# Optimization experiments

Hardware: AMD Instinct MI355X
Metric: run time of the kernel (lower is better)

Reference implementation:

```python
import jax, jax.numpy as jnp
import numpy as np

T = 200000  # stack depth
V = 130     # vocab_size == input_dim
H = 512     # hid_dim
L = 2       # n_layers


def setup_inputs() -> dict:
    key = jax.random.key(0)
    ks = jax.random.split(key, 24)
    s = 0.05
    inp = {
        "input": jax.random.normal(ks[0], (1, 1, V), jnp.float32),
        "prev_Val": jax.random.normal(ks[1], (T, V), jnp.float32),
        "prev_stg": jax.random.uniform(ks[2], (T,), jnp.float32),
        "prev_read": jax.random.normal(ks[3], (V,), jnp.float32),
        "prev_h": jax.random.normal(ks[4], (L, 1, H), jnp.float32) * 0.1,
        "prev_c": jax.random.normal(ks[5], (L, 1, H), jnp.float32) * 0.1,
        # LSTM layer 0 (pytorch layout: W_ih (4H, in), W_hh (4H, H), gates i,f,g,o)
        "W_ih0": jax.random.normal(ks[6], (4 * H, V), jnp.float32) * s,
        "W_hh0": jax.random.normal(ks[7], (4 * H, H), jnp.float32) * s,
        "b_ih0": jax.random.normal(ks[8], (4 * H,), jnp.float32) * s,
        "b_hh0": jax.random.normal(ks[9], (4 * H,), jnp.float32) * s,
        # LSTM layer 1
        "W_ih1": jax.random.normal(ks[10], (4 * H, H), jnp.float32) * s,
        "W_hh1": jax.random.normal(ks[11], (4 * H, H), jnp.float32) * s,
        "b_ih1": jax.random.normal(ks[12], (4 * H,), jnp.float32) * s,
        "b_hh1": jax.random.normal(ks[13], (4 * H,), jnp.float32) * s,
        # gate heads (original inits these to zeros; random here to exercise math)
        "Wd": jax.random.normal(ks[14], (H,), jnp.float32) * s,
        "Bd": jax.random.normal(ks[15], (), jnp.float32) * s,
        "Wu": jax.random.normal(ks[16], (H,), jnp.float32) * s,
        "Bu": jax.random.normal(ks[17], (), jnp.float32) * s,
        "Wv": jax.random.normal(ks[18], (H, V), jnp.float32) * s,
        "Bv": jax.random.normal(ks[19], (V,), jnp.float32) * s,
        "Wo": jax.random.normal(ks[20], (H, H), jnp.float32) * s,
        "Bo": jax.random.normal(ks[21], (H,), jnp.float32) * s,
    }
    return inp


def _lstm_cell(x, h, c, Wih, Whh, bih, bhh):
    # x: (1, in), h/c: (1, H)
    g = x @ Wih.T + h @ Whh.T + bih + bhh  # (1, 4H)
    i, f, gg, o = jnp.split(g, 4, axis=-1)
    c2 = jax.nn.sigmoid(f) * c + jax.nn.sigmoid(i) * jnp.tanh(gg)
    h2 = jax.nn.sigmoid(o) * jnp.tanh(c2)
    return h2, c2


def reference(input, prev_Val, prev_stg, prev_read, prev_h, prev_c,
              W_ih0, W_hh0, b_ih0, b_hh0, W_ih1, W_hh1, b_ih1, b_hh1,
              Wd, Bd, Wu, Bu, Wv, Bv, Wo, Bo):
    x = (input + prev_read)[0]  # (1, V), seq_len == 1, batch == 1
    h1, c1 = _lstm_cell(x, prev_h[0], prev_c[0], W_ih0, W_hh0, b_ih0, b_hh0)
    h2, c2 = _lstm_cell(h1, prev_h[1], prev_c[1], W_ih1, W_hh1, b_ih1, b_hh1)
    output = h2  # (1, H)

    dt = jax.nn.sigmoid(output @ Wd + Bd)[0]      # scalar push strength
    ut = jax.nn.sigmoid(output @ Wu + Bu)[0]      # scalar pop strength
    vt = jnp.tanh(output @ Wv + Bv)               # (1, V) pushed value
    ot = jnp.tanh(output @ Wo + Bo)               # (1, H) controller output

    Val = jnp.concatenate([prev_Val, vt], axis=0)  # (T+1, V)

    # pop pass (top -> bottom): stg[i] = max(0, prev_stg[i] - max(0, ut)); ut -= stg[i]
    def pop_step(u, s):
        sn = jnp.maximum(0.0, s - jnp.maximum(0.0, u))
        return u - sn, sn
    _, stg_popped = jax.lax.scan(pop_step, ut, prev_stg, reverse=True)
    stg = jnp.concatenate([stg_popped, dt[None]])  # (T+1,)

    # read pass (top -> bottom): coef = min(stg[i], max(0, read)); read -= stg[i]
    def read_step(r, s):
        coef = jnp.minimum(s, jnp.maximum(0.0, r))
        return r - s, coef
    _, coefs = jax.lax.scan(read_step, jnp.asarray(1.0, stg.dtype), stg, reverse=True)
    rt = coefs @ Val  # (V,)

    h_new = jnp.stack([h1, h2])  # (L, 1, H)
    c_new = jnp.stack([c1, c2])
    return ot, Val, stg, rt, h_new, c_new
```

## Files before the change

### kernel.cpp

```cpp
#include <hip/hip_runtime.h>

#define T_DEPTH 200000
#define V_DIM   130
#define H_DIM   512

#define OT_OFF   0
#define VAL_OFF  512
#define STG_OFF  26000642
#define RT_OFF   26200643
#define HN_OFF   26200773
#define CN_OFF   26201797

#define WS_DTUT  0
#define WS_H1    64
#define WS_C1    576
#define WS_H2    1088
#define WS_C2    1600

#define NV4 6500000
#define NS2 100000

static __device__ __forceinline__ float sigmoidf_(float x) {
  return 1.0f / (1.0f + expf(-x));
}

__global__ void k_bulk(const float4* __restrict__ val_in,
                       const float2* __restrict__ stg_in,
                       float* __restrict__ out) {
  const int NT = NV4 + NS2;
  float4* __restrict__ val_out = reinterpret_cast<float4*>(out + VAL_OFF);
  float2* __restrict__ stg_out = reinterpret_cast<float2*>(out + STG_OFF);
  int stride = gridDim.x * blockDim.x;
  for (int u = blockIdx.x * blockDim.x + threadIdx.x; u < NT; u += stride) {
    if (u < NV4) val_out[u] = val_in[u];
    else { int s = u - NV4; stg_out[s] = stg_in[s]; }
  }
}

static __device__ __forceinline__ void lstm_unit(
    const float* __restrict__ Wih, int in_dim,
    const float* __restrict__ x_a, const float* __restrict__ x_b,
    const float* __restrict__ Whh, const float* __restrict__ hprev,
    const float* __restrict__ bih, const float* __restrict__ bhh,
    const float* __restrict__ cprev, int j, int lane,
    float* __restrict__ h_ws, float* __restrict__ c_ws,
    float* __restrict__ h_out, float* __restrict__ c_out) {
  float pg[4];
#pragma unroll
  for (int q = 0; q < 4; ++q) {
    int row = q * H_DIM + j;
    const float* wr = Wih + row * in_dim;
    const float* wh = Whh + row * H_DIM;
    float acc = 0.f;
    if (x_b) {
      for (int c = lane; c < in_dim; c += 64) acc += wr[c] * (x_a[c] + x_b[c]);
    } else {
      for (int c = lane; c < in_dim; c += 64) acc += wr[c] * x_a[c];
    }
    for (int k = lane; k < H_DIM; k += 64) acc += wh[k] * hprev[k];
    for (int off = 32; off; off >>= 1) acc += __shfl_down(acc, off, 64);
    pg[q] = acc;
  }
  if (lane == 0) {
    float ig = sigmoidf_(pg[0] + bih[j] + bhh[j]);
    float fg = sigmoidf_(pg[1] + bih[H_DIM + j] + bhh[H_DIM + j]);
    float gg = tanhf(pg[2] + bih[2 * H_DIM + j] + bhh[2 * H_DIM + j]);
    float og = sigmoidf_(pg[3] + bih[3 * H_DIM + j] + bhh[3 * H_DIM + j]);
    float cn = fg * cprev[j] + ig * gg;
    float hn = og * tanhf(cn);
    h_ws[j] = hn; c_ws[j] = cn;
    h_out[j] = hn; c_out[j] = cn;
  }
}

__global__ void kL0(const float* __restrict__ Wih, const float* __restrict__ Whh,
                    const float* __restrict__ bih, const float* __restrict__ bhh,
                    const float* __restrict__ inp, const float* __restrict__ prd,
                    const float* __restrict__ hprev, const float* __restrict__ cprev,
                    float* __restrict__ ws, float* __restrict__ out) {
  int j = blockIdx.x * 4 + (threadIdx.x >> 6), lane = threadIdx.x & 63;
  lstm_unit(Wih, V_DIM, inp, prd, Whh, hprev, bih, bhh, cprev, j, lane,
            ws + WS_H1, ws + WS_C1, out + HN_OFF, out + CN_OFF);
}

__global__ void kL1(const float* __restrict__ Wih, const float* __restrict__ Whh,
                    const float* __restrict__ bih, const float* __restrict__ bhh,
                    const float* __restrict__ hprev, const float* __restrict__ cprev,
                    float* __restrict__ ws, float* __restrict__ out) {
  int j = blockIdx.x * 4 + (threadIdx.x >> 6), lane = threadIdx.x & 63;
  lstm_unit(Wih, H_DIM, ws + WS_H1, nullptr, Whh, hprev, bih, bhh, cprev, j, lane,
            ws + WS_H2, ws + WS_C2, out + HN_OFF + H_DIM, out + CN_OFF + H_DIM);
}

__global__ void kheads(const float* __restrict__ Wv, const float* __restrict__ Bv,
                       const float* __restrict__ Wo, const float* __restrict__ Bo,
                       const float* __restrict__ Wd, const float* __restrict__ Bd,
                       const float* __restrict__ Wu, const float* __restrict__ Bu,
                       float* __restrict__ ws, float* __restrict__ out) {
  int bid = blockIdx.x, tid = threadIdx.x;
  const float* h2 = ws + WS_H2;
  if (bid < 2) {
    int t = bid * 256 + tid;
    float a0 = 0.f, a1 = 0.f, a2 = 0.f, a3 = 0.f;
    for (int k = 0; k < H_DIM; k += 4) {
      a0 += h2[k]     * Wo[k * H_DIM + t];
      a1 += h2[k + 1] * Wo[(k + 1) * H_DIM + t];
      a2 += h2[k + 2] * Wo[(k + 2) * H_DIM + t];
      a3 += h2[k + 3] * Wo[(k + 3) * H_DIM + t];
    }
    out[OT_OFF + t] = tanhf(((a0 + a1) + (a2 + a3)) + Bo[t]);
  } else if (bid == 2) {
    if (tid < V_DIM) {
      float a0 = 0.f, a1 = 0.f, a2 = 0.f, a3 = 0.f;
      for (int k = 0; k < H_DIM; k += 4) {
        a0 += h2[k]     * Wv[k * V_DIM + tid];
        a1 += h2[k + 1] * Wv[(k + 1) * V_DIM + tid];
        a2 += h2[k + 2] * Wv[(k + 2) * V_DIM + tid];
        a3 += h2[k + 3] * Wv[(k + 3) * V_DIM + tid];
      }
      out[VAL_OFF + T_DEPTH * V_DIM + tid] = tanhf(((a0 + a1) + (a2 + a3)) + Bv[tid]);
    }
  } else {
    int wid = tid >> 6, lane = tid & 63;
    if (wid < 2) {
      const float* wv = (wid == 0) ? Wd : Wu;
      float acc = 0.f;
      for (int k = lane; k < H_DIM; k += 64) acc += h2[k] * wv[k];
      for (int off = 32; off; off >>= 1) acc += __shfl_down(acc, off, 64);
      if (lane == 0) {
        if (wid == 0) {
          float dt = sigmoidf_(acc + Bd[0]);
          ws[WS_DTUT + 0] = dt;
          out[STG_OFF + T_DEPTH] = dt;
        } else {
          ws[WS_DTUT + 1] = sigmoidf_(acc + Bu[0]);
        }
      }
    }
  }
}

__global__ void ktop(const float* __restrict__ prev_stg, const float* __restrict__ prev_val,
                     const float* __restrict__ ws, float* __restrict__ out) {
  int t = threadIdx.x;
  float dt = ws[WS_DTUT + 0];
  float u  = ws[WS_DTUT + 1];
  float r  = 1.0f;
  float acc = 0.f;
  {
    float coef = fminf(dt, fmaxf(0.f, r));
    if (t < V_DIM) acc += coef * out[VAL_OFF + T_DEPTH * V_DIM + t];
    r -= dt;
  }
  for (int i = T_DEPTH - 1; i >= 0; --i) {
    bool pop_active = (u > 0.f);
    if (!pop_active && r <= 0.f) break;
    float s  = prev_stg[i];
    float sn = fmaxf(0.f, s - fmaxf(0.f, u));
    u -= sn;
    if (pop_active && t == 0) out[STG_OFF + i] = sn;
    float coef = fminf(sn, fmaxf(0.f, r));
    r -= sn;
    if (coef > 0.f && t < V_DIM) acc += coef * prev_val[i * V_DIM + t];
  }
  if (t < V_DIM) out[RT_OFF + t] = acc;
}

extern "C" void kernel_launch(void* const* d_in, const int* in_sizes, int n_in,
                              void* d_out, int out_size, void* d_ws, size_t ws_size,
                              hipStream_t stream) {
  (void)in_sizes; (void)n_in; (void)out_size; (void)ws_size;
  const float* input     = (const float*)d_in[0];
  const float* prev_Val  = (const float*)d_in[1];
  const float* prev_stg  = (const float*)d_in[2];
  const float* prev_read = (const float*)d_in[3];
  const float* prev_h    = (const float*)d_in[4];
  const float* prev_c    = (const float*)d_in[5];
  const float* W_ih0 = (const float*)d_in[6];
  const float* W_hh0 = (const float*)d_in[7];
  const float* b_ih0 = (const float*)d_in[8];
  const float* b_hh0 = (const float*)d_in[9];
  const float* W_ih1 = (const float*)d_in[10];
  const float* W_hh1 = (const float*)d_in[11];
  const float* b_ih1 = (const float*)d_in[12];
  const float* b_hh1 = (const float*)d_in[13];
  const float* Wd = (const float*)d_in[14];
  const float* Bd = (const float*)d_in[15];
  const float* Wu = (const float*)d_in[16];
  const float* Bu = (const float*)d_in[17];
  const float* Wv = (const float*)d_in[18];
  const float* Bv = (const float*)d_in[19];
  const float* Wo = (const float*)d_in[20];
  const float* Bo = (const float*)d_in[21];

  float* out = (float*)d_out;
  float* ws  = (float*)d_ws;

  k_bulk<<<4096, 256, 0, stream>>>((const float4*)prev_Val, (const float2*)prev_stg, out);
  kL0<<<128, 256, 0, stream>>>(W_ih0, W_hh0, b_ih0, b_hh0, input, prev_read,
                               prev_h, prev_c, ws, out);
  kL1<<<128, 256, 0, stream>>>(W_ih1, W_hh1, b_ih1, b_hh1,
                               prev_h + H_DIM, prev_c + H_DIM, ws, out);
  kheads<<<4, 256, 0, stream>>>(Wv, Bv, Wo, Bo, Wd, Bd, Wu, Bu, ws, out);
  ktop<<<1, 192, 0, stream>>>(prev_stg, prev_Val, ws, out);
}
```

Before: 307.9 us.

## Fuse head and stack-scan kernels; unroll bulk copy with nontemporal stores

The bulk copy of the value stack now uses 1024 blocks, an 8-way unrolled loop and nontemporal stores, meant to raise memory-level parallelism and avoid polluting the cache. The separate heads and stack-scan kernels are merged into one tail kernel. Its last block computes dt and ut with shared-memory reductions, recomputes vt locally and then runs the pop/read scan, which removes one launch and a workspace round trip. The price is that one block redundantly recomputes the vt projection, adding serial latency before the scan starts.

After: 314.9 us. 2.3% more time.

```diff
diff --git a/kernel.cpp b/kernel.cpp
--- a/kernel.cpp
+++ b/kernel.cpp
@@ -11,7 +11,6 @@
 #define HN_OFF   26200773
 #define CN_OFF   26201797
 
-#define WS_DTUT  0
 #define WS_H1    64
 #define WS_C1    576
 #define WS_H2    1088
@@ -19,22 +18,46 @@
 
 #define NV4 6500000
 #define NS2 100000
+#define CB  1024
+
+typedef float f32x4 __attribute__((ext_vector_type(4)));
+typedef float f32x2 __attribute__((ext_vector_type(2)));
 
 static __device__ __forceinline__ float sigmoidf_(float x) {
   return 1.0f / (1.0f + expf(-x));
 }
 
-__global__ void k_bulk(const float4* __restrict__ val_in,
-                       const float2* __restrict__ stg_in,
-                       float* __restrict__ out) {
-  const int NT = NV4 + NS2;
-  float4* __restrict__ val_out = reinterpret_cast<float4*>(out + VAL_OFF);
-  float2* __restrict__ stg_out = reinterpret_cast<float2*>(out + STG_OFF);
-  int stride = gridDim.x * blockDim.x;
-  for (int u = blockIdx.x * blockDim.x + threadIdx.x; u < NT; u += stride) {
-    if (u < NV4) val_out[u] = val_in[u];
-    else { int s = u - NV4; stg_out[s] = stg_in[s]; }
-  }
+__global__ void k_bulk8(const f32x4* __restrict__ vin,
+                        const f32x2* __restrict__ sin2,
+                        float* __restrict__ out) {
+  f32x4* __restrict__ vout = reinterpret_cast<f32x4*>(out + VAL_OFF);
+  const int S = gridDim.x * blockDim.x;
+  const int w = blockIdx.x * blockDim.x + threadIdx.x;
+  int u = w;
+  for (; u + 7 * S < NV4; u += 8 * S) {
+    f32x4 a0 = vin[u];
+    f32x4 a1 = vin[u + S];
+    f32x4 a2 = vin[u + 2 * S];
+    f32x4 a3 = vin[u + 3 * S];
+    f32x4 a4 = vin[u + 4 * S];
+    f32x4 a5 = vin[u + 5 * S];
+    f32x4 a6 = vin[u + 6 * S];
+    f32x4 a7 = vin[u + 7 * S];
+    __builtin_nontemporal_store(a0, vout + u);
+    __builtin_nontemporal_store(a1, vout + u + S);
+    __builtin_nontemporal_store(a2, vout + u + 2 * S);
+    __builtin_nontemporal_store(a3, vout + u + 3 * S);
+    __builtin_nontemporal_store(a4, vout + u + 4 * S);
+    __builtin_nontemporal_store(a5, vout + u + 5 * S);
+    __builtin_nontemporal_store(a6, vout + u + 6 * S);
+    __builtin_nontemporal_store(a7, vout + u + 7 * S);
+  }
+  for (; u < NV4; u += S) {
+    f32x4 a = vin[u];
+    __builtin_nontemporal_store(a, vout + u);
+  }
+  f32x2* __restrict__ sout = reinterpret_cast<f32x2*>(out + STG_OFF);
+  for (int v = w; v < NS2; v += S) sout[v] = sin2[v];
 }
 
 static __device__ __forceinline__ void lstm_unit(
@@ -92,11 +115,12 @@
             ws + WS_H2, ws + WS_C2, out + HN_OFF + H_DIM, out + CN_OFF + H_DIM);
 }
 
-__global__ void kheads(const float* __restrict__ Wv, const float* __restrict__ Bv,
-                       const float* __restrict__ Wo, const float* __restrict__ Bo,
-                       const float* __restrict__ Wd, const float* __restrict__ Bd,
-                       const float* __restrict__ Wu, const float* __restrict__ Bu,
-                       float* __restrict__ ws, float* __restrict__ out) {
+__global__ void ktail(const float* __restrict__ Wv, const float* __restrict__ Bv,
+                      const float* __restrict__ Wo, const float* __restrict__ Bo,
+                      const float* __restrict__ Wd, const float* __restrict__ Bd,
+                      const float* __restrict__ Wu, const float* __restrict__ Bu,
+                      const float* __restrict__ prev_stg, const float* __restrict__ prev_val,
+                      const float* __restrict__ ws, float* __restrict__ out) {
   int bid = blockIdx.x, tid = threadIdx.x;
   const float* h2 = ws + WS_H2;
   if (bid < 2) {
@@ -121,49 +145,62 @@
       out[VAL_OFF + T_DEPTH * V_DIM + tid] = tanhf(((a0 + a1) + (a2 + a3)) + Bv[tid]);
     }
   } else {
-    int wid = tid >> 6, lane = tid & 63;
-    if (wid < 2) {
-      const float* wv = (wid == 0) ? Wd : Wu;
-      float acc = 0.f;
-      for (int k = lane; k < H_DIM; k += 64) acc += h2[k] * wv[k];
-      for (int off = 32; off; off >>= 1) acc += __shfl_down(acc, off, 64);
-      if (lane == 0) {
-        if (wid == 0) {
-          float dt = sigmoidf_(acc + Bd[0]);
-          ws[WS_DTUT + 0] = dt;
-          out[STG_OFF + T_DEPTH] = dt;
-        } else {
-          ws[WS_DTUT + 1] = sigmoidf_(acc + Bu[0]);
-        }
+    __shared__ float red[256];
+    __shared__ float s_dt, s_ut;
+    float pd = h2[tid] * Wd[tid] + h2[tid + 256] * Wd[tid + 256];
+    float pu = h2[tid] * Wu[tid] + h2[tid + 256] * Wu[tid + 256];
+    red[tid] = pd;
+    __syncthreads();
+    for (int s = 128; s; s >>= 1) {
+      if (tid < s) red[tid] += red[tid + s];
+      __syncthreads();
+    }
+    if (tid == 0) s_dt = sigmoidf_(red[0] + Bd[0]);
+    __syncthreads();
+    red[tid] = pu;
+    __syncthreads();
+    for (int s = 128; s; s >>= 1) {
+      if (tid < s) red[tid] += red[tid + s];
+      __syncthreads();
+    }
+    if (tid == 0) s_ut = sigmoidf_(red[0] + Bu[0]);
+    __syncthreads();
+    float dt = s_dt;
+    float u  = s_ut;
+
+    float vt_local = 0.f;
+    if (tid < V_DIM) {
+      float a0 = 0.f, a1 = 0.f, a2 = 0.f, a3 = 0.f;
+      for (int k = 0; k < H_DIM; k += 4) {
+        a0 += h2[k]     * Wv[k * V_DIM + tid];
+        a1 += h2[k + 1] * Wv[(k + 1) * V_DIM + tid];
+        a2 += h2[k + 2] * Wv[(k + 2) * V_DIM + tid];
+        a3 += h2[k + 3] * Wv[(k + 3) * V_DIM + tid];
       }
-    }
-  }
-}
-
-__global__ void ktop(const float* __restrict__ prev_stg, const float* __restrict__ prev_val,
-                     const float* __restrict__ ws, float* __restrict__ out) {
-  int t = threadIdx.x;
-  float dt = ws[WS_DTUT + 0];
-  float u  = ws[WS_DTUT + 1];
-  float r  = 1.0f;
-  float acc = 0.f;
-  {
-    float coef = fminf(dt, fmaxf(0.f, r));
-    if (t < V_DIM) acc += coef * out[VAL_OFF + T_DEPTH * V_DIM + t];
-    r -= dt;
-  }
-  for (int i = T_DEPTH - 1; i >= 0; --i) {
-    bool pop_active = (u > 0.f);
-    if (!pop_active && r <= 0.f) break;
-    float s  = prev_stg[i];
-    float sn = fmaxf(0.f, s - fmaxf(0.f, u));
-    u -= sn;
-    if (pop_active && t == 0) out[STG_OFF + i] = sn;
-    float coef = fminf(sn, fmaxf(0.f, r));
-    r -= sn;
-    if (coef > 0.f && t < V_DIM) acc += coef * prev_val[i * V_DIM + t];
-  }
-  if (t < V_DIM) out[RT_OFF + t] = acc;
+      vt_local = tanhf(((a0 + a1) + (a2 + a3)) + Bv[tid]);
+    }
+    if (tid == 0) out[STG_OFF + T_DEPTH] = dt;
+
+    float r = 1.0f;
+    float acc = 0.f;
+    {
+      float coef = fminf(dt, fmaxf(0.f, r));
+      if (tid < V_DIM) acc += coef * vt_local;
+      r -= dt;
+    }
+    for (int i = T_DEPTH - 1; i >= 0; --i) {
+      bool pop_active = (u > 0.f);
+      if (!pop_active && r <= 0.f) break;
+      float s  = prev_stg[i];
+      float sn = fmaxf(0.f, s - fmaxf(0.f, u));
+      u -= sn;
+      if (pop_active && tid == 0) out[STG_OFF + i] = sn;
+      float coef = fminf(sn, fmaxf(0.f, r));
+      r -= sn;
+      if (coef > 0.f && tid < V_DIM) acc += coef * prev_val[i * V_DIM + tid];
+    }
+    if (tid < V_DIM) out[RT_OFF + tid] = acc;
+  }
 }
 
 extern "C" void kernel_launch(void* const* d_in, const int* in_sizes, int n_in,
@@ -196,11 +233,11 @@
   float* out = (float*)d_out;
   float* ws  = (float*)d_ws;
 
-  k_bulk<<<4096, 256, 0, stream>>>((const float4*)prev_Val, (const float2*)prev_stg, out);
+  k_bulk8<<<CB, 256, 0, stream>>>((const f32x4*)prev_Val, (const f32x2*)prev_stg, out);
   kL0<<<128, 256, 0, stream>>>(W_ih0, W_hh0, b_ih0, b_hh0, input, prev_read,
                                prev_h, prev_c, ws, out);
   kL1<<<128, 256, 0, stream>>>(W_ih1, W_hh1, b_ih1, b_hh1,
                                prev_h + H_DIM, prev_c + H_DIM, ws, out);
-  kheads<<<4, 256, 0, stream>>>(Wv, Bv, Wo, Bo, Wd, Bd, Wu, Bu, ws, out);
-  ktop<<<1, 192, 0, stream>>>(prev_stg, prev_Val, ws, out);
-}
+  ktail<<<4, 256, 0, stream>>>(Wv, Bv, Wo, Bo, Wd, Bd, Wu, Bu,
+                               prev_stg, prev_Val, ws, out);
+}
```
